# Optimization experiments

Hardware: AMD Instinct MI355X
Metric: run time of the kernel (lower is better)

The kernel has to match this reference:

```python
import jax, jax.numpy as jnp
import numpy as np

B, S, F = 512, 512, 128   # batch, seq_len, facts_size (= querry_size)
H1, H2 = 80, 40
PAD = float(-2**32 + 1)


def setup_inputs() -> dict:
    key = jax.random.key(0)
    ks = jax.random.split(key, 12)
    inp = {
        "query": jax.random.normal(ks[0], (B, F), jnp.float32),
        "facts": jax.random.normal(ks[1], (B, S, F), jnp.float32),
        "mask": jax.random.randint(ks[2], (B, S), 0, 2, jnp.int32),
        # mlp1: querry_size -> facts_size
        "W1": jax.random.normal(ks[3], (F, F), jnp.float32) / np.sqrt(F),
        "b1": jnp.zeros((F,), jnp.float32),
        # PReLU alpha (per-feature, init zeros)
        "alpha": jnp.zeros((F,), jnp.float32),
        # mlp2: 4*F -> 80
        "W2": jax.random.normal(ks[4], (4 * F, H1), jnp.float32) / np.sqrt(4 * F),
        "b2": jnp.zeros((H1,), jnp.float32),
        # mlp3: 80 -> 40
        "W3": jax.random.normal(ks[5], (H1, H2), jnp.float32) / np.sqrt(H1),
        "b3": jnp.zeros((H2,), jnp.float32),
        # mlp4: 40 -> 1
        "W4": jax.random.normal(ks[6], (H2, 1), jnp.float32) / np.sqrt(H2),
        "b4": jnp.zeros((1,), jnp.float32),
    }
    return inp


def reference(query, facts, mask, W1, b1, alpha, W2, b2, W3, b3, W4, b4):
    # mlp1 + PReLU on the query
    q = query @ W1 + b1                                   # [B, F]
    q = jnp.where(q >= 0, q, alpha * q)                   # PReLU, alpha per-feature
    # broadcast query over sequence (tile+reshape in the original)
    qs = jnp.broadcast_to(q[:, None, :], (q.shape[0], S, F))  # [B, S, F]
    din = jnp.concatenate([qs, facts, qs - facts, qs * facts], axis=-1)  # [B,S,4F]
    h1 = jax.nn.sigmoid(din @ W2 + b2)                    # [B, S, 80]
    h2 = jax.nn.sigmoid(h1 @ W3 + b3)                     # [B, S, 40]
    scores = (h2 @ W4 + b4)[..., 0][:, None, :]           # [B, 1, S]
    key_masks = (mask == 1)[:, None, :]                   # [B, 1, S]
    scores = jnp.where(key_masks, scores, PAD)
    scores = jax.nn.softmax(scores, axis=-1)              # softmax over seq
    out = jnp.einsum("bqs,bsf->bqf", scores, facts)       # [B, 1, F]  (mode SUM)
    return out
```

## Files before the change

### kernel.cpp

```cpp
#include <hip/hip_runtime.h>
#include <hip/hip_bf16.h>

typedef __bf16 bf16x8 __attribute__((ext_vector_type(8)));
typedef float  f32x4  __attribute__((ext_vector_type(4)));

#define WBT_STRIDE 136
#define H1_STRIDE  104
#define W3T_STRIDE 104

#define LOAD_CT(av, rl)                                                         \
    {                                                                           \
        const float* p0 = &fb[(size_t)(wave * 64 + (rl)) * 128 + qd * 8];       \
        _Pragma("unroll")                                                       \
        for (int kc = 0; kc < 4; ++kc) {                                        \
            av[kc][0] = *(const f32x4*)(p0 + kc * 32);                          \
            av[kc][1] = *(const f32x4*)(p0 + kc * 32 + 4);                      \
        }                                                                       \
    }

#define CONV_AF(af, av)                                                         \
    _Pragma("unroll")                                                           \
    for (int kc = 0; kc < 4; ++kc)                                              \
        _Pragma("unroll")                                                       \
        for (int i = 0; i < 8; ++i)                                             \
            af[kc][i] = (__bf16)((i < 4) ? av[kc][0][i] : av[kc][1][i - 4]);

#define SCORE_CT(af, tile)                                                      \
    {                                                                           \
         \
        _Pragma("unroll")                                                       \
        for (int ct = 0; ct < 5; ++ct) {                                        \
            f32x4 acc = {0.f, 0.f, 0.f, 0.f};                                   \
            _Pragma("unroll")                                                   \
            for (int kc = 0; kc < 4; ++kc) {                                    \
                bf16x8 bfr = *(const bf16x8*)&WbT[(ct * 16 + m) * WBT_STRIDE + kc * 32 + qd * 8]; \
                acc = __builtin_amdgcn_mfma_f32_16x16x32_bf16(af[kc], bfr, acc, 0, 0, 0); \
            }                                                                   \
            const int col = ct * 16 + m;   \
            const float qc = qcs[col];                                          \
            _Pragma("unroll")                                                   \
            for (int r = 0; r < 4; ++r) {                                       \
                float x = acc[r] + qc;                                          \
                float h = __builtin_amdgcn_rcpf(1.0f + __expf(-x));             \
                h1w[(qd * 4 + r) * H1_STRIDE + col] = (__bf16)h;                \
            }                                                                   \
        }                                                                       \
        asm volatile("s_waitcnt lgkmcnt(0)" ::: "memory");    \
           \
        bf16x8 a2[3];                                                           \
        _Pragma("unroll")                                                       \
        for (int kc = 0; kc < 3; ++kc)                                          \
            a2[kc] = *(const bf16x8*)&h1w[m * H1_STRIDE + kc * 32 + qd * 8];    \
        float sco = 0.f;                                                        \
        _Pragma("unroll")                                                       \
        for (int ct = 0; ct < 3; ++ct) {                                        \
            f32x4 acc2 = {0.f, 0.f, 0.f, 0.f};                                  \
            _Pragma("unroll")                                                   \
            for (int kc = 0; kc < 3; ++kc) {                                    \
                bf16x8 bfr = *(const bf16x8*)&W3T[(ct * 16 + m) * W3T_STRIDE + kc * 32 + qd * 8]; \
                acc2 = __builtin_amdgcn_mfma_f32_16x16x32_bf16(bfr, a2[kc], acc2, 0, 0, 0); \
            }                                                                   \
            _Pragma("unroll")                                                   \
            for (int r = 0; r < 4; ++r) {                                       \
                const int j = ct * 16 + qd * 4 + r;                             \
                float h2 = __builtin_amdgcn_rcpf(1.0f + __expf(-(acc2[r] + b3s[j]))); \
                sco = fmaf(h2, w4s[j], sco);                                    \
            }                                                                   \
        }                                                                       \
        sco += __shfl_xor(sco, 16);                                             \
        sco += __shfl_xor(sco, 32);                                             \
         \
        const float pmv = (((tile) * 16 + m) < cnt) ? __expf(sco) : 0.f;        \
        Zl += pmv;                                                              \
        if (qd == 0) pmall[wave * 64 + (tile) * 16 + m] = pmv;                  \
    }

__global__ __launch_bounds__(512, 2)
void attn_fused(const float* __restrict__ query,
                const float* __restrict__ facts,
                const int*   __restrict__ mask,
                const float* __restrict__ W1, const float* __restrict__ b1,
                const float* __restrict__ alpha,
                const float* __restrict__ W2, const float* __restrict__ b2,
                const float* __restrict__ W3, const float* __restrict__ b3,
                const float* __restrict__ W4,
                float* __restrict__ out)
{
    __shared__ __align__(16) __bf16 WbT[80 * WBT_STRIDE];
    __shared__ __align__(16) __bf16 W3T[48 * W3T_STRIDE];
    __shared__ __align__(16) __bf16 h1all[128 * H1_STRIDE];
    __shared__ float qy[128], qs[128], qcs[80];
    __shared__ float qpart[4][128], qcp[4][80];
    __shared__ float w4s[48], b3s[48];
    __shared__ float outw[8 * 128];
    __shared__ __align__(16) float pmall[8 * 64];
    __shared__ __align__(4) unsigned char cidx8[8 * 64];
    __shared__ float Zw[8];

    const int b = blockIdx.x, t = threadIdx.x;
    const int wave = t >> 6, lane = t & 63, qd = lane >> 4, m = lane & 15;
    const float* fb = facts + (size_t)b * (512 * 128);
    const int*   mb = mask + b * 512;

    const int mvl = mb[wave * 64 + lane];
    const unsigned long long bal = __ballot(mvl == 1);
    const int cnt = __popcll(bal);
    cidx8[wave * 64 + lane] = 0;
    asm volatile("s_waitcnt lgkmcnt(0)" ::: "memory");
    if (mvl == 1) {
        const int rank = __popcll(bal & ((1ull << lane) - 1ull));
        cidx8[wave * 64 + rank] = (unsigned char)lane;
    }
    asm volatile("s_waitcnt lgkmcnt(0)" ::: "memory");
    const int rl0 = cidx8[wave * 64 +  0 + m];
    const int rl1 = cidx8[wave * 64 + 16 + m];
    const int rl2 = cidx8[wave * 64 + 32 + m];
    const int rl3 = cidx8[wave * 64 + 48 + m];

    f32x4 av0[4][2], av1[4][2];
    LOAD_CT(av0, rl0)
    if (cnt > 16) LOAD_CT(av1, rl1)

    if (t < 128) qy[t] = query[b * 128 + t];
    for (int e = t; e < 48 * 96; e += 512) {
        int j = e / 96, k = e % 96;
        W3T[j * W3T_STRIDE + k] = (j < 40 && k < 80) ? (__bf16)W3[k * 40 + j]
                                                     : (__bf16)0.0f;
    }
    for (int e = t; e < 128 * 16; e += 512) {
        int r = e >> 4, c = 80 + (e & 15);
        h1all[r * H1_STRIDE + c] = (__bf16)0.0f;
    }
    if (t < 48) { w4s[t] = (t < 40) ? W4[t] : 0.f; b3s[t] = (t < 40) ? b3[t] : 0.f; }
    __syncthreads();

    {
        int j = t & 127, kh = t >> 7;
        float acc = (kh == 0) ? b1[j] : 0.f;
        const float* w1p = W1 + (kh * 32) * 128 + j;
        #pragma unroll 8
        for (int k = 0; k < 32; ++k) acc = fmaf(qy[kh * 32 + k], w1p[k * 128], acc);
        qpart[kh][j] = acc;
    }
    __syncthreads();
    if (t < 128) {
        float s = (qpart[0][t] + qpart[1][t]) + (qpart[2][t] + qpart[3][t]);
        qs[t] = (s >= 0.f) ? s : alpha[t] * s;
    }
    __syncthreads();

    if (t < 320) {
        int jj = t % 80, hh = t / 80;
        float acc = (hh == 0) ? b2[jj] : 0.f;
        #pragma unroll 8
        for (int k = hh * 32; k < hh * 32 + 32; ++k)
            acc = fmaf(qs[k], W2[k * 80 + jj] + W2[(256 + k) * 80 + jj], acc);
        qcp[hh][jj] = acc;
    }
    for (int e = t; e < 128 * 80; e += 512) {
        int k = e / 80, n = e - k * 80;
        float w = W2[(128 + k) * 80 + n] - W2[(256 + k) * 80 + n]
                + qs[k] * W2[(384 + k) * 80 + n];
        WbT[n * WBT_STRIDE + k] = (__bf16)w;
    }
    __syncthreads();
    if (t < 80) qcs[t] = (qcp[0][t] + qcp[1][t]) + (qcp[2][t] + qcp[3][t]);
    __syncthreads();

    __bf16* h1w = &h1all[wave * 16 * H1_STRIDE];

    float Zl = 0.f;
    bf16x8 af[4];

    CONV_AF(af, av0)
    if (cnt > 32) LOAD_CT(av0, rl2)
    SCORE_CT(af, 0)
    if (cnt > 16) {
        CONV_AF(af, av1)
        if (cnt > 48) LOAD_CT(av1, rl3)
        SCORE_CT(af, 1)
    }
    if (cnt > 32) {
        CONV_AF(af, av0)
        SCORE_CT(af, 2)
    }
    if (cnt > 48) {
        CONV_AF(af, av1)
        SCORE_CT(af, 3)
    }

    asm volatile("s_waitcnt lgkmcnt(0)" ::: "memory");
    float oA = 0.f, oB = 0.f;
    {
        const float* fw = fb + (size_t)(wave * 64) * 128;
        const float* pmw = &pmall[wave * 64];
        const unsigned int* ci4p = (const unsigned int*)&cidx8[wave * 64];
        const int ng = (cnt + 3) >> 2;
        #pragma unroll 4
        for (int g = 0; g < ng; ++g) {
            const f32x4 p4 = *(const f32x4*)&pmw[g * 4];
            const unsigned int c4 = ci4p[g];
            const int r0 = c4 & 255, r1 = (c4 >> 8) & 255;
            const int r2 = (c4 >> 16) & 255, r3 = c4 >> 24;
            oA = fmaf(p4[0], fw[r0 * 128 + lane], oA);
            oB = fmaf(p4[0], fw[r0 * 128 + 64 + lane], oB);
            oA = fmaf(p4[1], fw[r1 * 128 + lane], oA);
            oB = fmaf(p4[1], fw[r1 * 128 + 64 + lane], oB);
            oA = fmaf(p4[2], fw[r2 * 128 + lane], oA);
            oB = fmaf(p4[2], fw[r2 * 128 + 64 + lane], oB);
            oA = fmaf(p4[3], fw[r3 * 128 + lane], oA);
            oB = fmaf(p4[3], fw[r3 * 128 + 64 + lane], oB);
        }
        outw[wave * 128 + lane] = oA;
        outw[wave * 128 + 64 + lane] = oB;
    }

    #pragma unroll
    for (int d = 1; d < 16; d <<= 1) Zl += __shfl_xor(Zl, d);
    if (lane == 0) Zw[wave] = Zl;
    __syncthreads();

    if (t < 128) {
        float v = 0.f, Z = 0.f;
        #pragma unroll
        for (int w = 0; w < 8; ++w) { v += outw[w * 128 + t]; Z += Zw[w]; }
        out[b * 128 + t] = v / Z;
    }
}

extern "C" void kernel_launch(void* const* d_in, const int* in_sizes, int n_in,
                              void* d_out, int out_size, void* d_ws, size_t ws_size,
                              hipStream_t stream) {
    (void)in_sizes; (void)n_in; (void)d_ws; (void)ws_size; (void)out_size;
    const float* query = (const float*)d_in[0];
    const float* facts = (const float*)d_in[1];
    const int*   mask  = (const int*)d_in[2];
    const float* W1 = (const float*)d_in[3];
    const float* b1 = (const float*)d_in[4];
    const float* al = (const float*)d_in[5];
    const float* W2 = (const float*)d_in[6];
    const float* b2 = (const float*)d_in[7];
    const float* W3 = (const float*)d_in[8];
    const float* b3 = (const float*)d_in[9];
    const float* W4 = (const float*)d_in[10];
    const float* b4 = (const float*)d_in[11];
    (void)b4;
    attn_fused<<<dim3(512), dim3(512), 0, stream>>>(
        query, facts, mask, W1, b1, al, W2, b2, W3, b3, W4, (float*)d_out);
}
```

Measured before the change: 231.5 us.

## Reuse register-held facts for weighted sum via per-wave LDS slab

The softmax-weighted sum of facts now happens inside each tile's scoring step. The fp32 fact rows already held in registers are staged through a per-wave LDS slab and accumulated with the tile's probabilities, instead of re-gathering the fact rows from global memory in a separate pass. The h1 scratch buffer is aliased onto that slab, which cuts shared memory, and the prefetch of the next tile's facts is shifted one tile later. This removes a second global read of facts in exchange for extra LDS writes, reads and waitcnt barriers inside the per-tile chain, and it holds fewer tiles in flight.

```diff
diff --git a/kernel.cpp b/kernel.cpp
--- a/kernel.cpp
+++ b/kernel.cpp
@@ -7,6 +7,7 @@
 #define WBT_STRIDE 136
 #define H1_STRIDE  104
 #define W3T_STRIDE 104
+#define SLAB_F32   68
 
 #define LOAD_CT(av, rl)                                                         \
     {                                                                           \
@@ -25,9 +26,10 @@
         for (int i = 0; i < 8; ++i)                                             \
             af[kc][i] = (__bf16)((i < 4) ? av[kc][0][i] : av[kc][1][i - 4]);
 
-#define SCORE_CT(af, tile)                                                      \
+#define CHAIN_CT(af, av, tile)                                                  \
     {                                                                           \
-         \
+        asm volatile("" ::: "memory");                                          \
+             \
         _Pragma("unroll")                                                       \
         for (int ct = 0; ct < 5; ++ct) {                                        \
             f32x4 acc = {0.f, 0.f, 0.f, 0.f};                                   \
@@ -46,11 +48,23 @@
             }                                                                   \
         }                                                                       \
         asm volatile("s_waitcnt lgkmcnt(0)" ::: "memory");    \
+        bf16x8 a2[3];                                                           \
+        a2[0] = *(const bf16x8*)&h1w[m * H1_STRIDE + qd * 8];                   \
+        a2[1] = *(const bf16x8*)&h1w[m * H1_STRIDE + 32 + qd * 8];              \
+        if (qd < 2) {                                                           \
+            a2[2] = *(const bf16x8*)&h1w[m * H1_STRIDE + 64 + qd * 8];          \
+        } else {                                                                \
+            _Pragma("unroll")                                                   \
+            for (int i = 0; i < 8; ++i) a2[2][i] = (__bf16)0.0f;                \
+        }                                                                       \
+        asm volatile("" ::: "memory");                                          \
+         \
+        _Pragma("unroll")                                                       \
+        for (int kc = 0; kc < 2; ++kc)                                          \
+            _Pragma("unroll")                                                   \
+            for (int h = 0; h < 2; ++h)                                         \
+                *(f32x4*)&sw[m * SLAB_F32 + qd * 8 + kc * 32 + h * 4] = av[kc][h]; \
            \
-        bf16x8 a2[3];                                                           \
-        _Pragma("unroll")                                                       \
-        for (int kc = 0; kc < 3; ++kc)                                          \
-            a2[kc] = *(const bf16x8*)&h1w[m * H1_STRIDE + kc * 32 + qd * 8];    \
         float sco = 0.f;                                                        \
         _Pragma("unroll")                                                       \
         for (int ct = 0; ct < 3; ++ct) {                                        \
@@ -73,6 +87,27 @@
         const float pmv = (((tile) * 16 + m) < cnt) ? __expf(sco) : 0.f;        \
         Zl += pmv;                                                              \
         if (qd == 0) pmall[wave * 64 + (tile) * 16 + m] = pmv;                  \
+        asm volatile("s_waitcnt lgkmcnt(0)" ::: "memory");                      \
+                         \
+        _Pragma("unroll")                                                       \
+        for (int s = 0; s < 16; ++s) {                                          \
+            const float p = pmw[(tile) * 16 + s];                               \
+            oA = fmaf(p, sw[s * SLAB_F32 + lane], oA);                          \
+        }                                                                       \
+        asm volatile("" ::: "memory");                                          \
+         \
+        _Pragma("unroll")                                                       \
+        for (int kc = 2; kc < 4; ++kc)                                          \
+            _Pragma("unroll")                                                   \
+            for (int h = 0; h < 2; ++h)                                         \
+                *(f32x4*)&sw[m * SLAB_F32 + qd * 8 + (kc - 2) * 32 + h * 4] = av[kc][h]; \
+        asm volatile("s_waitcnt lgkmcnt(0)" ::: "memory");                      \
+                                             \
+        _Pragma("unroll")                                                       \
+        for (int s = 0; s < 16; ++s) {                                          \
+            const float p = pmw[(tile) * 16 + s];                               \
+            oB = fmaf(p, sw[s * SLAB_F32 + lane], oB);                          \
+        }                                                                       \
     }
 
 __global__ __launch_bounds__(512, 2)
@@ -88,13 +123,13 @@
 {
     __shared__ __align__(16) __bf16 WbT[80 * WBT_STRIDE];
     __shared__ __align__(16) __bf16 W3T[48 * W3T_STRIDE];
-    __shared__ __align__(16) __bf16 h1all[128 * H1_STRIDE];
+    __shared__ __align__(16) float slabf[8 * 16 * SLAB_F32];
     __shared__ float qy[128], qs[128], qcs[80];
     __shared__ float qpart[4][128], qcp[4][80];
     __shared__ float w4s[48], b3s[48];
     __shared__ float outw[8 * 128];
-    __shared__ __align__(16) float pmall[8 * 64];
-    __shared__ __align__(4) unsigned char cidx8[8 * 64];
+    __shared__ float pmall[8 * 64];
+    __shared__ unsigned char cidx8[8 * 64];
     __shared__ float Zw[8];
 
     const int b = blockIdx.x, t = threadIdx.x;
@@ -119,17 +154,12 @@
 
     f32x4 av0[4][2], av1[4][2];
     LOAD_CT(av0, rl0)
-    if (cnt > 16) LOAD_CT(av1, rl1)
 
     if (t < 128) qy[t] = query[b * 128 + t];
     for (int e = t; e < 48 * 96; e += 512) {
         int j = e / 96, k = e % 96;
         W3T[j * W3T_STRIDE + k] = (j < 40 && k < 80) ? (__bf16)W3[k * 40 + j]
                                                      : (__bf16)0.0f;
-    }
-    for (int e = t; e < 128 * 16; e += 512) {
-        int r = e >> 4, c = 80 + (e & 15);
-        h1all[r * H1_STRIDE + c] = (__bf16)0.0f;
     }
     if (t < 48) { w4s[t] = (t < 40) ? W4[t] : 0.f; b3s[t] = (t < 40) ? b3[t] : 0.f; }
     __syncthreads();
@@ -167,54 +197,33 @@
     if (t < 80) qcs[t] = (qcp[0][t] + qcp[1][t]) + (qcp[2][t] + qcp[3][t]);
     __syncthreads();
 
-    __bf16* h1w = &h1all[wave * 16 * H1_STRIDE];
-
-    float Zl = 0.f;
+    __bf16* h1w = (__bf16*)&slabf[wave * 16 * SLAB_F32];
+    float*  sw  = &slabf[wave * 16 * SLAB_F32];
+    const float* pmw = &pmall[wave * 64];
+
+    float Zl = 0.f, oA = 0.f, oB = 0.f;
     bf16x8 af[4];
 
     CONV_AF(af, av0)
-    if (cnt > 32) LOAD_CT(av0, rl2)
-    SCORE_CT(af, 0)
+    if (cnt > 16) LOAD_CT(av1, rl1)
+    CHAIN_CT(af, av0, 0)
     if (cnt > 16) {
         CONV_AF(af, av1)
-        if (cnt > 48) LOAD_CT(av1, rl3)
-        SCORE_CT(af, 1)
+        if (cnt > 32) LOAD_CT(av0, rl2)
+        CHAIN_CT(af, av1, 1)
     }
     if (cnt > 32) {
         CONV_AF(af, av0)
-        SCORE_CT(af, 2)
+        if (cnt > 48) LOAD_CT(av1, rl3)
+        CHAIN_CT(af, av0, 2)
     }
     if (cnt > 48) {
         CONV_AF(af, av1)
-        SCORE_CT(af, 3)
-    }
-
-    asm volatile("s_waitcnt lgkmcnt(0)" ::: "memory");
-    float oA = 0.f, oB = 0.f;
-    {
-        const float* fw = fb + (size_t)(wave * 64) * 128;
-        const float* pmw = &pmall[wave * 64];
-        const unsigned int* ci4p = (const unsigned int*)&cidx8[wave * 64];
-        const int ng = (cnt + 3) >> 2;
-        #pragma unroll 4
-        for (int g = 0; g < ng; ++g) {
-            const f32x4 p4 = *(const f32x4*)&pmw[g * 4];
-            const unsigned int c4 = ci4p[g];
-            const int r0 = c4 & 255, r1 = (c4 >> 8) & 255;
-            const int r2 = (c4 >> 16) & 255, r3 = c4 >> 24;
-            oA = fmaf(p4[0], fw[r0 * 128 + lane], oA);
-            oB = fmaf(p4[0], fw[r0 * 128 + 64 + lane], oB);
-            oA = fmaf(p4[1], fw[r1 * 128 + lane], oA);
-            oB = fmaf(p4[1], fw[r1 * 128 + 64 + lane], oB);
-            oA = fmaf(p4[2], fw[r2 * 128 + lane], oA);
-            oB = fmaf(p4[2], fw[r2 * 128 + 64 + lane], oB);
-            oA = fmaf(p4[3], fw[r3 * 128 + lane], oA);
-            oB = fmaf(p4[3], fw[r3 * 128 + 64 + lane], oB);
-        }
-        outw[wave * 128 + lane] = oA;
-        outw[wave * 128 + 64 + lane] = oB;
-    }
-
+        CHAIN_CT(af, av1, 3)
+    }
+
+    outw[wave * 128 + lane] = oA;
+    outw[wave * 128 + 64 + lane] = oB;
     #pragma unroll
     for (int d = 1; d < 16; d <<= 1) Zl += __shfl_xor(Zl, d);
     if (lane == 0) Zw[wave] = Zl;
```

Result: faster. 224.8 us (-2.9%).
